# Performance work log

Hardware: AMD Instinct MI355X
Metric: run time of the kernel (lower is better)

Reference implementation:

```python
import jax, jax.numpy as jnp
import numpy as np

B, C, H, W = 1024, 256, 19, 19
CH, CV = 32, 48  # c_head, c_val
B_AVG = 9.0


def setup_inputs() -> dict:
    key = jax.random.key(0)
    ks = jax.random.split(key, 14)
    s = 0.05
    d = {}
    d["x"] = jax.random.normal(ks[0], (B, C, H, W), jnp.float32)
    d["conv_w"] = jax.random.normal(ks[1], (CH, C), jnp.float32) * s  # 1x1 conv, no bias
    d["fc1_w"] = jax.random.normal(ks[2], (CV, 3 * CH), jnp.float32) * s
    d["fc1_b"] = jax.random.normal(ks[3], (CV,), jnp.float32) * s
    d["fc2_w"] = jax.random.normal(ks[4], (1, CV), jnp.float32) * s
    d["fc2_b"] = jax.random.normal(ks[5], (1,), jnp.float32) * s
    d["fc3_w"] = jax.random.normal(ks[6], (CV, 3 * CH), jnp.float32) * s
    d["fc3_b"] = jax.random.normal(ks[7], (CV,), jnp.float32) * s
    d["sc_w"] = jax.random.normal(ks[8], (1, CV), jnp.float32) * s
    d["sc_b"] = jax.random.normal(ks[9], (1,), jnp.float32) * s
    d["fc4_w"] = jax.random.normal(ks[10], (CV, 3 * CH + 1), jnp.float32) * s
    d["fc4_b"] = jax.random.normal(ks[11], (CV,), jnp.float32) * s
    d["fc5_w"] = jax.random.normal(ks[12], (1, CV), jnp.float32) * s
    d["fc5_b"] = jax.random.normal(ks[13], (1,), jnp.float32) * s
    return d


def reference(x, conv_w, fc1_w, fc1_b, fc2_w, fc2_b, fc3_w, fc3_b,
              sc_w, sc_b, fc4_w, fc4_b, fc5_w, fc5_b):
    # 1x1 conv (bias=False) == channel-mixing matmul
    V = jnp.einsum('bchw,oc->bohw', x, conv_w)  # [B, CH, H, W]

    # GlobalPooling (value_head=False branch: real spatial max)
    mean1 = V.mean(axis=(2, 3))                         # [B, CH]
    mean2 = mean1 * ((V.shape[2] - B_AVG) / 10.0)       # [B, CH]
    mx = V.max(axis=(2, 3))                             # [B, CH]
    Vp = jnp.concatenate([mean1, mean2, mx], axis=1)    # [B, 3*CH]

    # game outcome head
    game_out = jnp.tanh(jax.nn.relu(Vp @ fc1_w.T + fc1_b) @ fc2_w.T + fc2_b)  # [B, 1]

    # scaling factor head
    scaling = jax.nn.relu(Vp @ fc3_w.T + fc3_b) @ sc_w.T + sc_b  # [B, 1]

    # distance logits: the original loops over 41 d values; here the d axis is batched.
    dvals = jnp.arange(-20, 21, dtype=jnp.float32)               # [41]
    base = Vp @ fc4_w[:, :-1].T + fc4_b                          # [B, CV]
    d_term = dvals[:, None] * fc4_w[:, -1][None, :]              # [41, CV]
    h = jax.nn.relu(base[:, None, :] + d_term[None, :, :])       # [B, 41, CV]
    logits = h @ fc5_w[0] + fc5_b[0]                             # [B, 41]

    probs = jax.nn.softmax(logits * scaling, axis=1)             # [B, 41]
    return (game_out, probs)
```

## Files before the change

kernel.cpp:

```cpp
#include <hip/hip_runtime.h>
#include <math.h>

#define C_IN   256
#define C_HEAD 32
#define HW     361
#define NTHR   384
#define CV     48
#define WSTR   264
#define NCHUNK 8
#define FLIM   (C_IN * HW - 4)
#define GSTR   552
#define WVSTR  2208
#define XSF    (6 * WVSTR)

typedef __attribute__((ext_vector_type(8))) short bf16x8;
typedef __attribute__((ext_vector_type(4))) float f32x4;

static __device__ __forceinline__ unsigned short f2bf(float f) {
    unsigned int u = __builtin_bit_cast(unsigned int, f);
    u += 0x7fffu + ((u >> 16) & 1u);
    return (unsigned short)(u >> 16);
}

__global__ __launch_bounds__(NTHR, 3) void vh_fused(
    const float* __restrict__ x,
    const float* __restrict__ conv_w,
    const float* __restrict__ fc1_w, const float* __restrict__ fc1_b,
    const float* __restrict__ fc2_w, const float* __restrict__ fc2_b,
    const float* __restrict__ fc3_w, const float* __restrict__ fc3_b,
    const float* __restrict__ sc_w,  const float* __restrict__ sc_b,
    const float* __restrict__ fc4_w, const float* __restrict__ fc4_b,
    const float* __restrict__ fc5_w, const float* __restrict__ fc5_b,
    float* __restrict__ out, int B)
{
    const int b    = blockIdx.x;
    const int tid  = threadIdx.x;
    const int wave = tid >> 6;
    const int lane = tid & 63;
    const int l15  = lane & 15;
    const int g    = lane >> 4;

    __shared__ __align__(16) unsigned short wtT[C_HEAD * WSTR];
    __shared__ __align__(16) float xs[XSF];
    __shared__ float lds_psum[C_HEAD][6];
    __shared__ float lds_pmax[C_HEAD][6];
    __shared__ float vp[3 * C_HEAD];
    __shared__ float base_l[CV], dco_l[CV], f5_l[CV];

    for (int i = tid; i < C_HEAD * C_IN; i += NTHR) {
        int o = i >> 8, c = i & 255;
        wtT[o * WSTR + c] = f2bf(conv_w[i]);
    }
    __syncthreads();

    f32x4 acc[4][2];
    #pragma unroll
    for (int mi = 0; mi < 4; ++mi)
        #pragma unroll
        for (int n = 0; n < 2; ++n)
            acc[mi][n] = (f32x4){0.f, 0.f, 0.f, 0.f};

    const float* __restrict__ xb = x + (size_t)b * (C_IN * HW);

    const int thbase = g * (8 * HW) + wave * 64 + l15 * 4;
    const int wb_w   = wave * WVSTR + g * GSTR + l15 * 4;
    const int wb_r   = wave * WVSTR + g * GSTR + l15;
    const int ep     = l15 & 7;

    float4 va[9], vb[9];

    auto issue = [&](int t, float4 (&bank)[9]) {
        #pragma unroll
        for (int e = 0; e < 8; ++e) {
            int F = thbase + ((t * 32 + e) * HW - (e & 3));
            if (t == NCHUNK - 1 && e == 7)
                F = (F > FLIM) ? FLIM : F;
            bank[e] = *(const float4*)(xb + F);
        }
        int Ft = (t * 32 + g * 8 + ep) * HW + wave * 64 + 64 - (ep & 3);
        if (t == NCHUNK - 1) Ft = (Ft > FLIM) ? FLIM : Ft;
        bank[8] = *(const float4*)(xb + Ft);
    };

    auto write_lds = [&](float4 (&bank)[9]) {
        #pragma unroll
        for (int e = 0; e < 8; ++e)
            *(float4*)&xs[wb_w + e * 68] = bank[e];
        if (l15 < 8)
            *(float4*)&xs[wave * WVSTR + g * GSTR + ep * 68 + 64] = bank[8];
    };

    auto compute = [&](int t) {
        bf16x8 wf0 = *(const bf16x8*)&wtT[(     l15) * WSTR + t * 32 + g * 8];
        bf16x8 wf1 = *(const bf16x8*)&wtT[(16 + l15) * WSTR + t * 32 + g * 8];
        #pragma unroll
        for (int mi = 0; mi < 4; ++mi) {
            float af[8];
            #pragma unroll
            for (int e = 0; e < 8; ++e)
                af[e] = xs[wb_r + e * 68 + mi * 16 + (e & 3)];
            unsigned u0, u1, u2, u3;
            asm("v_cvt_pk_bf16_f32 %0, %1, %2" : "=v"(u0) : "v"(af[0]), "v"(af[1]));
            asm("v_cvt_pk_bf16_f32 %0, %1, %2" : "=v"(u1) : "v"(af[2]), "v"(af[3]));
            asm("v_cvt_pk_bf16_f32 %0, %1, %2" : "=v"(u2) : "v"(af[4]), "v"(af[5]));
            asm("v_cvt_pk_bf16_f32 %0, %1, %2" : "=v"(u3) : "v"(af[6]), "v"(af[7]));
            uint4 up = make_uint4(u0, u1, u2, u3);
            bf16x8 a = __builtin_bit_cast(bf16x8, up);
            acc[mi][0] = __builtin_amdgcn_mfma_f32_16x16x32_bf16(a, wf0, acc[mi][0], 0, 0, 0);
            acc[mi][1] = __builtin_amdgcn_mfma_f32_16x16x32_bf16(a, wf1, acc[mi][1], 0, 0, 0);
        }
    };

    issue(0, va);
    issue(1, vb);
    #pragma unroll
    for (int t = 0; t < NCHUNK; ++t) {
        if ((t & 1) == 0) {
            write_lds(va);
            if (t + 2 < NCHUNK) issue(t + 2, va);
        } else {
            write_lds(vb);
            if (t + 2 < NCHUNK) issue(t + 2, vb);
        }
        compute(t);
    }

    float s[2]  = {0.f, 0.f};
    float mx[2] = {-3.0e38f, -3.0e38f};
    #pragma unroll
    for (int n = 0; n < 2; ++n) {
        #pragma unroll
        for (int mi = 0; mi < 4; ++mi) {
            #pragma unroll
            for (int r = 0; r < 4; ++r) {
                int pp = wave * 64 + mi * 16 + g * 4 + r;
                float v = acc[mi][n][r];
                if (pp < HW) { s[n] += v; mx[n] = fmaxf(mx[n], v); }
            }
        }
        s[n] += __shfl_xor(s[n], 16, 64);
        s[n] += __shfl_xor(s[n], 32, 64);
        mx[n] = fmaxf(mx[n], __shfl_xor(mx[n], 16, 64));
        mx[n] = fmaxf(mx[n], __shfl_xor(mx[n], 32, 64));
    }
    if (lane < 32) {
        lds_psum[lane][wave] = (lane < 16) ? s[0] : s[1];
        lds_pmax[lane][wave] = (lane < 16) ? mx[0] : mx[1];
    }
    __syncthreads();

    if (tid < C_HEAD) {
        float ss = 0.f, mm = -3.0e38f;
        #pragma unroll
        for (int w = 0; w < 6; ++w) { ss += lds_psum[tid][w]; mm = fmaxf(mm, lds_pmax[tid][w]); }
        float mean1 = ss * (1.0f / (float)HW);
        vp[tid]              = mean1;
        vp[C_HEAD + tid]     = mean1 * ((19.0f - 9.0f) * 0.1f);
        vp[2 * C_HEAD + tid] = mm;
    }
    __syncthreads();

    if (wave == 0) {
        const int j = lane;
        float h1 = 0.f, h3 = 0.f;
        if (j < CV) {
            float a1 = fc1_b[j], a3 = fc3_b[j], a4 = fc4_b[j];
            #pragma unroll
            for (int k = 0; k < 96; ++k) {
                float v = vp[k];
                a1 = fmaf(v, fc1_w[j * 96 + k], a1);
                a3 = fmaf(v, fc3_w[j * 96 + k], a3);
                a4 = fmaf(v, fc4_w[j * 97 + k], a4);
            }
            h1 = fmaxf(a1, 0.f) * fc2_w[j];
            h3 = fmaxf(a3, 0.f) * sc_w[j];
            base_l[j] = a4;
            dco_l[j]  = fc4_w[j * 97 + 96];
            f5_l[j]   = fc5_w[j];
        }
        float s1 = h1, s3 = h3;
        #pragma unroll
        for (int off = 32; off > 0; off >>= 1) {
            s1 += __shfl_xor(s1, off, 64);
            s3 += __shfl_xor(s3, off, 64);
        }
        float game = tanhf(s1 + fc2_b[0]);
        float scal = s3 + sc_b[0];
        if (lane == 0) out[b] = game;

        float z = -3.0e38f;
        if (lane < 41) {
            float dval = (float)(lane - 20);
            float lg = fc5_b[0];
            #pragma unroll
            for (int jj = 0; jj < CV; ++jj) {
                float t2 = fmaf(dval, dco_l[jj], base_l[jj]);
                t2 = fmaxf(t2, 0.f);
                lg = fmaf(t2, f5_l[jj], lg);
            }
            z = lg * scal;
        }
        float mz = z;
        #pragma unroll
        for (int off = 32; off > 0; off >>= 1) mz = fmaxf(mz, __shfl_xor(mz, off, 64));
        float e = (lane < 41) ? expf(z - mz) : 0.f;
        float se = e;
        #pragma unroll
        for (int off = 32; off > 0; off >>= 1) se += __shfl_xor(se, off, 64);
        if (lane < 41) out[B + b * 41 + lane] = e / se;
    }
}

extern "C" void kernel_launch(void* const* d_in, const int* in_sizes, int n_in,
                              void* d_out, int out_size, void* d_ws, size_t ws_size,
                              hipStream_t stream) {
    const float* x      = (const float*)d_in[0];
    const float* conv_w = (const float*)d_in[1];
    const float* fc1_w  = (const float*)d_in[2];
    const float* fc1_b  = (const float*)d_in[3];
    const float* fc2_w  = (const float*)d_in[4];
    const float* fc2_b  = (const float*)d_in[5];
    const float* fc3_w  = (const float*)d_in[6];
    const float* fc3_b  = (const float*)d_in[7];
    const float* sc_w   = (const float*)d_in[8];
    const float* sc_b   = (const float*)d_in[9];
    const float* fc4_w  = (const float*)d_in[10];
    const float* fc4_b  = (const float*)d_in[11];
    const float* fc5_w  = (const float*)d_in[12];
    const float* fc5_b  = (const float*)d_in[13];
    float* out = (float*)d_out;

    int B = in_sizes[0] / (C_IN * HW);

    vh_fused<<<dim3(B), dim3(NTHR), 0, stream>>>(
        x, conv_w, fc1_w, fc1_b, fc2_w, fc2_b, fc3_w, fc3_b,
        sc_w, sc_b, fc4_w, fc4_b, fc5_w, fc5_b, out, B);
}
```

Before: 92.10 us.

## Stage x tile in LDS as bf16, single-buffer prefetch, raise occupancy target

Converts the fp32 x tile to bf16 before writing it to shared memory, which halves the LDS footprint and the write traffic, and moves the conversion from the read path to the write path. The register double-buffer is replaced by a single register bank prefetching one chunk ahead, and launch_bounds is raised from 3 to 5 blocks per CU. The goal is more resident blocks per CU to hide global-load latency on this memory-bound kernel. In exchange, the shallower prefetch depth exposes more latency per block, and the 16-bit LDS reads and shift/or packing add ALU work.

```diff
diff --git a/kernel.cpp b/kernel.cpp
--- a/kernel.cpp
+++ b/kernel.cpp
@@ -9,9 +9,9 @@
 #define WSTR   264
 #define NCHUNK 8
 #define FLIM   (C_IN * HW - 4)
-#define GSTR   552
-#define WVSTR  2208
-#define XSF    (6 * WVSTR)
+#define GSH    560
+#define WVSH   2240
+#define XSH    (6 * WVSH)
 
 typedef __attribute__((ext_vector_type(8))) short bf16x8;
 typedef __attribute__((ext_vector_type(4))) float f32x4;
@@ -22,7 +22,7 @@
     return (unsigned short)(u >> 16);
 }
 
-__global__ __launch_bounds__(NTHR, 3) void vh_fused(
+__global__ __launch_bounds__(NTHR, 5) void vh_fused(
     const float* __restrict__ x,
     const float* __restrict__ conv_w,
     const float* __restrict__ fc1_w, const float* __restrict__ fc1_b,
@@ -41,7 +41,7 @@
     const int g    = lane >> 4;
 
     __shared__ __align__(16) unsigned short wtT[C_HEAD * WSTR];
-    __shared__ __align__(16) float xs[XSF];
+    __shared__ __align__(16) unsigned short xs[XSH];
     __shared__ float lds_psum[C_HEAD][6];
     __shared__ float lds_pmax[C_HEAD][6];
     __shared__ float vp[3 * C_HEAD];
@@ -63,13 +63,12 @@
     const float* __restrict__ xb = x + (size_t)b * (C_IN * HW);
 
     const int thbase = g * (8 * HW) + wave * 64 + l15 * 4;
-    const int wb_w   = wave * WVSTR + g * GSTR + l15 * 4;
-    const int wb_r   = wave * WVSTR + g * GSTR + l15;
+    const int wb     = wave * WVSH + g * GSH;
     const int ep     = l15 & 7;
 
-    float4 va[9], vb[9];
-
-    auto issue = [&](int t, float4 (&bank)[9]) {
+    float4 bank[9];
+
+    auto issue = [&](int t) {
         #pragma unroll
         for (int e = 0; e < 8; ++e) {
             int F = thbase + ((t * 32 + e) * HW - (e & 3));
@@ -82,12 +81,20 @@
         bank[8] = *(const float4*)(xb + Ft);
     };
 
-    auto write_lds = [&](float4 (&bank)[9]) {
-        #pragma unroll
-        for (int e = 0; e < 8; ++e)
-            *(float4*)&xs[wb_w + e * 68] = bank[e];
-        if (l15 < 8)
-            *(float4*)&xs[wave * WVSTR + g * GSTR + ep * 68 + 64] = bank[8];
+    auto write_lds = [&]() {
+        #pragma unroll
+        for (int e = 0; e < 8; ++e) {
+            unsigned lo, hi;
+            asm("v_cvt_pk_bf16_f32 %0, %1, %2" : "=v"(lo) : "v"(bank[e].x), "v"(bank[e].y));
+            asm("v_cvt_pk_bf16_f32 %0, %1, %2" : "=v"(hi) : "v"(bank[e].z), "v"(bank[e].w));
+            *(uint2*)&xs[wb + e * 68 + l15 * 4] = make_uint2(lo, hi);
+        }
+        if (l15 < 8) {
+            unsigned lo, hi;
+            asm("v_cvt_pk_bf16_f32 %0, %1, %2" : "=v"(lo) : "v"(bank[8].x), "v"(bank[8].y));
+            asm("v_cvt_pk_bf16_f32 %0, %1, %2" : "=v"(hi) : "v"(bank[8].z), "v"(bank[8].w));
+            *(uint2*)&xs[wb + ep * 68 + 64] = make_uint2(lo, hi);
+        }
     };
 
     auto compute = [&](int t) {
@@ -95,33 +102,26 @@
         bf16x8 wf1 = *(const bf16x8*)&wtT[(16 + l15) * WSTR + t * 32 + g * 8];
         #pragma unroll
         for (int mi = 0; mi < 4; ++mi) {
-            float af[8];
+            unsigned af[8];
             #pragma unroll
             for (int e = 0; e < 8; ++e)
-                af[e] = xs[wb_r + e * 68 + mi * 16 + (e & 3)];
-            unsigned u0, u1, u2, u3;
-            asm("v_cvt_pk_bf16_f32 %0, %1, %2" : "=v"(u0) : "v"(af[0]), "v"(af[1]));
-            asm("v_cvt_pk_bf16_f32 %0, %1, %2" : "=v"(u1) : "v"(af[2]), "v"(af[3]));
-            asm("v_cvt_pk_bf16_f32 %0, %1, %2" : "=v"(u2) : "v"(af[4]), "v"(af[5]));
-            asm("v_cvt_pk_bf16_f32 %0, %1, %2" : "=v"(u3) : "v"(af[6]), "v"(af[7]));
-            uint4 up = make_uint4(u0, u1, u2, u3);
+                af[e] = (unsigned)xs[wb + e * 68 + mi * 16 + l15 + (e & 3)];
+            uint4 up;
+            up.x = af[0] | (af[1] << 16);
+            up.y = af[2] | (af[3] << 16);
+            up.z = af[4] | (af[5] << 16);
+            up.w = af[6] | (af[7] << 16);
             bf16x8 a = __builtin_bit_cast(bf16x8, up);
             acc[mi][0] = __builtin_amdgcn_mfma_f32_16x16x32_bf16(a, wf0, acc[mi][0], 0, 0, 0);
             acc[mi][1] = __builtin_amdgcn_mfma_f32_16x16x32_bf16(a, wf1, acc[mi][1], 0, 0, 0);
         }
     };
 
-    issue(0, va);
-    issue(1, vb);
+    issue(0);
     #pragma unroll
     for (int t = 0; t < NCHUNK; ++t) {
-        if ((t & 1) == 0) {
-            write_lds(va);
-            if (t + 2 < NCHUNK) issue(t + 2, va);
-        } else {
-            write_lds(vb);
-            if (t + 2 < NCHUNK) issue(t + 2, vb);
-        }
+        write_lds();
+        if (t + 1 < NCHUNK) issue(t + 1);
         compute(t);
     }
 
```

After: 98.49 us. 1.07x slower.
